# Optimization experiments

Measured on AMD Instinct MI355X. Metric: run time of the kernel, lower is better.

## Reference

```python
import jax, jax.numpy as jnp
import numpy as np

B, H, NQ, NK, D = 2, 16, 4096, 4096, 64


def _attn_with_lse(q, k, v, scale):
    # q: [B,H,p,d], k: [B,H,s,d], v: [B,H,s,dv]
    s = jnp.einsum('bhqd,bhkd->bhqk', q, k) * scale
    lse = jax.nn.logsumexp(s, axis=-1, keepdims=True)  # [B,H,p,1]
    p = jnp.exp(s - lse)
    o = jnp.einsum('bhqk,bhkd->bhqd', p, v)
    return o, lse


def setup_inputs() -> dict:
    key = jax.random.key(0)
    k1, k2, k3 = jax.random.split(key, 3)
    return {
        'query': jax.random.normal(k1, (B, H, NQ, D), dtype=jnp.float32),
        'key': jax.random.normal(k2, (B, H, NK, D), dtype=jnp.float32),
        'value': jax.random.normal(k3, (B, H, NK, D), dtype=jnp.float32),
        'n_query_groups': 4,
        'n_key_groups': 4,
    }


def reference(query, key, value, n_query_groups, n_key_groups):
    b, h, nq, d = query.shape
    nk = key.shape[2]
    m, n = int(n_query_groups), int(n_key_groups)
    scale = d ** (-0.5)
    pq, pk = nq // m, nk // n  # group sizes n_gp
    c0, c1 = m // 2, n // 2   # center groups c_gp

    # representative query/key blocks
    q_gp = query[:, :, c0 * pq:(c0 + 1) * pq, :]              # [B,H,pq,d]
    k_gp = key[:, :, c1 * pk:(c1 + 1) * pk, :]                # [B,H,pk,d]
    # value chunks concatenated on feature dim (zero-padding of q/k in the
    # original leaves the dot products unchanged, so we skip it)
    v_gp = value.reshape(b, h, n, pk, d).transpose(0, 1, 3, 2, 4).reshape(b, h, pk, n * d)
    attn_gp, lse_gp = _attn_with_lse(q_gp, k_gp, v_gp, scale)  # [B,H,pq,n*d], [B,H,pq,1]

    # sample one key per key group (torch uses random.randint; fixed to 0 here)
    k_picked = 0
    k_sample = key[:, :, k_picked::pk, :]                      # [B,H,n,d]
    w = jnp.einsum('bhqd,bhnd->bhqn', query, k_sample)         # [B,H,nq,n]
    w_gps = w.reshape(b, h, m, pq, n)
    norm_gps = jnp.linalg.norm(w_gps, axis=-2)                 # [B,H,m,n]
    s_gps = norm_gps / norm_gps[:, :, c0, c1][:, :, None, None]

    v_sum = value.reshape(b, h, n, pk, d).sum(axis=3)          # [B,H,n,d]
    om = jnp.maximum(1.0 - s_gps, 0.0)                         # clamp(1-s, min=0)
    num_part1 = om[:, :, :, :, None, None] * v_sum[:, :, None, :, None, :]  # [B,H,m,n,1,d]
    den_part1 = (om * pk)[:, :, :, :, None, None]              # [B,H,m,n,1,1]

    lse_exp = jnp.exp(lse_gp)                                  # [B,H,pq,1]
    unnorm = lse_exp * attn_gp                                 # [B,H,pq,n*d]
    attn_gps = unnorm.reshape(b, h, pq, n, d).transpose(0, 1, 3, 2, 4)  # [B,H,n,pq,d]
    num_part2 = s_gps[:, :, :, :, None, None] * attn_gps[:, :, None, :, :, :]  # [B,H,m,n,pq,d]
    den_part2 = s_gps[:, :, :, :, None, None] * lse_exp[:, :, None, None, :, :]  # [B,H,m,n,pq,1]

    num_agg = (num_part1 + num_part2).sum(axis=3)              # [B,H,m,pq,d]
    den_agg = (den_part1 + den_part2).sum(axis=3)              # [B,H,m,pq,1]

    attn = (num_agg / den_agg).reshape(b, h, nq, d)
    lse = jnp.log(den_agg).reshape(b, h, nq, 1)
    return attn, lse
```

## Files before the change

### kernel.cpp

```cpp
#include <hip/hip_runtime.h>
#include <hip/hip_bf16.h>


#define BH_TOT 32
#define SEQ    4096
#define DIM    64
#define PQ     1024

#define QB_OFF 34816u
#define KB_OFF (QB_OFF + 4u*1024u*1024u)
#define VB_OFF (KB_OFF + 4u*1024u*1024u)
#define WS_NEED (VB_OFF + 16u*1024u*1024u)
#define WS_NEED_FB 34816u

#define QSCALE 0.1803368801111204f

typedef __attribute__((ext_vector_type(8))) short bf16x8;
typedef __attribute__((ext_vector_type(4))) short bf16x4;
typedef __attribute__((ext_vector_type(4))) float f32x4;
typedef __attribute__((ext_vector_type(4))) _Float16 f16x4;
typedef __attribute__((ext_vector_type(8))) _Float16 f16x8;

__device__ __forceinline__ short f2bf(float x) {
    unsigned u = __float_as_uint(x);
    u = u + 0x7fffu + ((u >> 16) & 1u);
    return (short)(u >> 16);
}
__device__ __forceinline__ float bf2f(unsigned short h) {
    return __uint_as_float(((unsigned)h) << 16);
}

__global__ __launch_bounds__(256) void prep_norm2(
    const float* __restrict__ query, const float* __restrict__ key,
    float* __restrict__ ws)
{
    __shared__ float ksm[4][64];
    __shared__ float wsum[4][16];
    const int t = threadIdx.x;
    const int bh = blockIdx.x >> 2, gi = blockIdx.x & 3;
    if (t < 64) ws[512 + blockIdx.x * 64 + t] = 0.f;
    ksm[t >> 6][t & 63] = key[((size_t)bh * SEQ + (size_t)(t >> 6) * PQ) * DIM + (t & 63)];
    __syncthreads();
    const int wv = t >> 6, lane = t & 63, c = lane & 15, hi = lane >> 4;
    bf16x8 bb0, bb1;
#pragma unroll
    for (int j = 0; j < 8; ++j) {
        bb0[j] = (c < 4) ? f2bf(ksm[c][hi * 8 + j]) : (short)0;
        bb1[j] = (c < 4) ? f2bf(ksm[c][32 + hi * 8 + j]) : (short)0;
    }
    float acc0 = 0.f, acc1 = 0.f, acc2 = 0.f, acc3 = 0.f;
    const float* qbase = query + ((size_t)bh * SEQ + (size_t)gi * PQ) * DIM;
    for (int it = 0; it < 16; ++it) {
        const int row = (wv * 16 + it) * 16 + c;
        const float* qp = qbase + (size_t)row * 64 + hi * 8;
        float4 a0 = *(const float4*)qp;
        float4 a1 = *(const float4*)(qp + 4);
        float4 a2 = *(const float4*)(qp + 32);
        float4 a3 = *(const float4*)(qp + 36);
        bf16x8 qa0, qa1;
        qa0[0] = f2bf(a0.x); qa0[1] = f2bf(a0.y); qa0[2] = f2bf(a0.z); qa0[3] = f2bf(a0.w);
        qa0[4] = f2bf(a1.x); qa0[5] = f2bf(a1.y); qa0[6] = f2bf(a1.z); qa0[7] = f2bf(a1.w);
        qa1[0] = f2bf(a2.x); qa1[1] = f2bf(a2.y); qa1[2] = f2bf(a2.z); qa1[3] = f2bf(a2.w);
        qa1[4] = f2bf(a3.x); qa1[5] = f2bf(a3.y); qa1[6] = f2bf(a3.z); qa1[7] = f2bf(a3.w);
        f32x4 s = (f32x4){0.f, 0.f, 0.f, 0.f};
        s = __builtin_amdgcn_mfma_f32_16x16x32_bf16(qa0, bb0, s, 0, 0, 0);
        s = __builtin_amdgcn_mfma_f32_16x16x32_bf16(qa1, bb1, s, 0, 0, 0);
        acc0 += s[0] * s[0]; acc1 += s[1] * s[1];
        acc2 += s[2] * s[2]; acc3 += s[3] * s[3];
    }
    float asum = acc0 + acc1 + acc2 + acc3;
    asum += __shfl_xor(asum, 16);
    asum += __shfl_xor(asum, 32);
    if (lane < 16) wsum[wv][lane] = asum;
    __syncthreads();
    if (t < 4) ws[bh * 16 + gi * 4 + t] = wsum[0][t] + wsum[1][t] + wsum[2][t] + wsum[3][t];
}

__global__ __launch_bounds__(256) void conv_qk(
    const float* __restrict__ query, const float* __restrict__ key,
    char* __restrict__ wsb)
{
    const int t = threadIdx.x;
    if (blockIdx.x < 512) {
        const int bh = blockIdx.x >> 4, qt = blockIdx.x & 15;
#pragma unroll
        for (int i = 0; i < 2; ++i) {
            const int sid = t + i * 256;
            const int mt = sid >> 7, kh = (sid >> 6) & 1, lane = sid & 63;
            const int c = lane & 15, hi = lane >> 4;
            const float* p = query + ((size_t)bh * SEQ + 2048 + qt * 64 + mt * 16 + c) * DIM
                             + kh * 32 + hi * 8;
            float4 a = *(const float4*)p, b = *(const float4*)(p + 4);
            bf16x8 h;
            h[0] = f2bf(a.x * QSCALE); h[1] = f2bf(a.y * QSCALE);
            h[2] = f2bf(a.z * QSCALE); h[3] = f2bf(a.w * QSCALE);
            h[4] = f2bf(b.x * QSCALE); h[5] = f2bf(b.y * QSCALE);
            h[6] = f2bf(b.z * QSCALE); h[7] = f2bf(b.w * QSCALE);
            const size_t fidx = ((size_t)(bh * 16 + qt) * 4 + mt) * 2 + kh;
            *(bf16x8*)(wsb + QB_OFF + fidx * 1024 + lane * 16) = h;
        }
    } else {
        const int b2 = blockIdx.x - 512;
        const int bh = b2 >> 4, kc = b2 & 15;
#pragma unroll
        for (int i = 0; i < 2; ++i) {
            const int sid = t + i * 256;
            const int kh = sid >> 8, nt = (sid >> 6) & 3, lane = sid & 63;
            const int c = lane & 15, hi = lane >> 4;
            const float* p = key + ((size_t)bh * SEQ + 2048 + kc * 64 + nt * 16 + c) * DIM
                             + kh * 32 + hi * 8;
            float4 a = *(const float4*)p, b = *(const float4*)(p + 4);
            bf16x8 h;
            h[0] = f2bf(a.x); h[1] = f2bf(a.y); h[2] = f2bf(a.z); h[3] = f2bf(a.w);
            h[4] = f2bf(b.x); h[5] = f2bf(b.y); h[6] = f2bf(b.z); h[7] = f2bf(b.w);
            const size_t fidx = ((size_t)(bh * 16 + kc) * 2 + kh) * 4 + nt;
            *(bf16x8*)(wsb + KB_OFF + fidx * 1024 + lane * 16) = h;
        }
    }
}

__global__ __launch_bounds__(256) void conv_v(
    const float* __restrict__ value, char* __restrict__ wsb, float* __restrict__ ws)
{
    __shared__ float Ls[64][68];
    __shared__ float ps[4][64];
    const int t = threadIdx.x;
    const int blk = blockIdx.x;
    const int bh = blk >> 6, gj = (blk >> 4) & 3, kc = blk & 15;
    const float* src = value + ((size_t)bh * SEQ + gj * PQ + kc * 64) * DIM;
#pragma unroll
    for (int i = 0; i < 4; ++i) {
        const int u = t + i * 256;
        const int row = u >> 4, c4 = (u & 15) * 4;
        *(float4*)&Ls[row][c4] = *(const float4*)(src + row * 64 + c4);
    }
    __syncthreads();
    {
        const int d = t & 63, rg = t >> 6;
        float s = 0.f;
#pragma unroll
        for (int i = 0; i < 16; ++i) s += Ls[rg * 16 + i][d];
        ps[rg][d] = s;
    }
    __syncthreads();
    if (t < 64) {
        float tot = ps[0][t] + ps[1][t] + ps[2][t] + ps[3][t];
        atomicAdd(&ws[512 + bh * 256 + gj * 64 + t], tot);
    }
#pragma unroll
    for (int i = 0; i < 2; ++i) {
        const int sid = t + i * 256;
        const int pl = sid >> 8, dt = (sid >> 6) & 3, lane = sid & 63;
        const int c = lane & 15, hi = lane >> 4;
        f16x8 h;
#pragma unroll
        for (int s2 = 0; s2 < 2; ++s2)
#pragma unroll
            for (int j = 0; j < 4; ++j)
                h[s2 * 4 + j] = (_Float16)Ls[(pl * 2 + s2) * 16 + hi * 4 + j][dt * 16 + c];
        const size_t off = ((((size_t)(bh * 4 + gj) * 32 + kc * 2 + pl) * 4 + dt) * 64 + lane) * 16;
        *(f16x8*)(wsb + VB_OFF + off) = h;
    }
}

__global__ __launch_bounds__(256, 4) void kattn3(
    const char* __restrict__ wsb, float* __restrict__ out)
{
    __shared__ union {
        _Float16 P[2][32][72];
        float Uf[32][257];
    } lds;
    __shared__ float Llds[32];

    const int blk = blockIdx.x;
    const int bh = blk >> 5, qt = blk & 31;
    const int t = threadIdx.x;
    const int w = t >> 6, lane = t & 63;
    const int c = lane & 15, hi = lane >> 4;

    bf16x8 aq[2][2];
#pragma unroll
    for (int qt2 = 0; qt2 < 2; ++qt2) {
        const int s = qt * 2 + qt2;
        const size_t fr = ((size_t)(bh * 16 + (s >> 2)) * 4 + (s & 3)) * 2;
        aq[qt2][0] = *(const bf16x8*)(wsb + QB_OFF + fr * 1024 + lane * 16);
        aq[qt2][1] = *(const bf16x8*)(wsb + QB_OFF + (fr + 1) * 1024 + lane * 16);
    }
    const char* kb = wsb + KB_OFF + ((size_t)(bh * 16) * 8) * 1024 + (size_t)w * 1024 + lane * 16;
    const char* vb = wsb + VB_OFF + ((size_t)(bh * 4 + w) * 128) * 1024 + lane * 16;

    f32x4 Uacc[2][4];
#pragma unroll
    for (int mt = 0; mt < 2; ++mt)
#pragma unroll
        for (int dt = 0; dt < 4; ++dt)
            Uacc[mt][dt] = (f32x4){0.f, 0.f, 0.f, 0.f};
    f32x4 Lacc[2];
    Lacc[0] = (f32x4){0.f, 0.f, 0.f, 0.f};
    Lacc[1] = (f32x4){0.f, 0.f, 0.f, 0.f};
    const f16x4 kOnes = (f16x4){(_Float16)1.f, (_Float16)1.f, (_Float16)1.f, (_Float16)1.f};

    for (int kc = 0; kc < 16; ++kc) {
        const int buf = kc & 1;
        bf16x8 bk0 = *(const bf16x8*)(kb + (size_t)kc * 8192);
        bf16x8 bk1 = *(const bf16x8*)(kb + (size_t)kc * 8192 + 4096);
        f32x4 sacc[2];
#pragma unroll
        for (int qt2 = 0; qt2 < 2; ++qt2) {
            f32x4 s = (f32x4){0.f, 0.f, 0.f, 0.f};
            s = __builtin_amdgcn_mfma_f32_16x16x32_bf16(bk0, aq[qt2][0], s, 0, 0, 0);
            s = __builtin_amdgcn_mfma_f32_16x16x32_bf16(bk1, aq[qt2][1], s, 0, 0, 0);
            sacc[qt2] = s;
        }
#pragma unroll
        for (int qt2 = 0; qt2 < 2; ++qt2) {
            f16x4 ph;
#pragma unroll
            for (int r = 0; r < 4; ++r)
                ph[r] = (_Float16)__builtin_amdgcn_exp2f(sacc[qt2][r]);
            *(f16x4*)&lds.P[buf][qt2 * 16 + c][w * 16 + hi * 4] = ph;
        }
        const char* vcb = vb + (size_t)kc * 8192;
        f16x8 vfa0 = *(const f16x8*)(vcb);
        f16x8 vfa1 = *(const f16x8*)(vcb + 1024);
        f16x8 vfa2 = *(const f16x8*)(vcb + 2048);
        f16x8 vfa3 = *(const f16x8*)(vcb + 3072);
        f16x8 vfb0 = *(const f16x8*)(vcb + 4096);
        f16x8 vfb1 = *(const f16x8*)(vcb + 5120);
        f16x8 vfb2 = *(const f16x8*)(vcb + 6144);
        f16x8 vfb3 = *(const f16x8*)(vcb + 7168);
        __syncthreads();
        f16x4 ap[2][4];
#pragma unroll
        for (int mt = 0; mt < 2; ++mt)
#pragma unroll
            for (int kt = 0; kt < 4; ++kt)
                ap[mt][kt] = *(const f16x4*)&lds.P[buf][mt * 16 + c][kt * 16 + hi * 4];
#pragma unroll
        for (int mt = 0; mt < 2; ++mt) {
            Uacc[mt][0] = __builtin_amdgcn_mfma_f32_16x16x16f16(ap[mt][0], __builtin_shufflevector(vfa0, vfa0, 0, 1, 2, 3), Uacc[mt][0], 0, 0, 0);
            Uacc[mt][1] = __builtin_amdgcn_mfma_f32_16x16x16f16(ap[mt][0], __builtin_shufflevector(vfa1, vfa1, 0, 1, 2, 3), Uacc[mt][1], 0, 0, 0);
            Uacc[mt][2] = __builtin_amdgcn_mfma_f32_16x16x16f16(ap[mt][0], __builtin_shufflevector(vfa2, vfa2, 0, 1, 2, 3), Uacc[mt][2], 0, 0, 0);
            Uacc[mt][3] = __builtin_amdgcn_mfma_f32_16x16x16f16(ap[mt][0], __builtin_shufflevector(vfa3, vfa3, 0, 1, 2, 3), Uacc[mt][3], 0, 0, 0);
            Uacc[mt][0] = __builtin_amdgcn_mfma_f32_16x16x16f16(ap[mt][1], __builtin_shufflevector(vfa0, vfa0, 4, 5, 6, 7), Uacc[mt][0], 0, 0, 0);
            Uacc[mt][1] = __builtin_amdgcn_mfma_f32_16x16x16f16(ap[mt][1], __builtin_shufflevector(vfa1, vfa1, 4, 5, 6, 7), Uacc[mt][1], 0, 0, 0);
            Uacc[mt][2] = __builtin_amdgcn_mfma_f32_16x16x16f16(ap[mt][1], __builtin_shufflevector(vfa2, vfa2, 4, 5, 6, 7), Uacc[mt][2], 0, 0, 0);
            Uacc[mt][3] = __builtin_amdgcn_mfma_f32_16x16x16f16(ap[mt][1], __builtin_shufflevector(vfa3, vfa3, 4, 5, 6, 7), Uacc[mt][3], 0, 0, 0);
            Uacc[mt][0] = __builtin_amdgcn_mfma_f32_16x16x16f16(ap[mt][2], __builtin_shufflevector(vfb0, vfb0, 0, 1, 2, 3), Uacc[mt][0], 0, 0, 0);
            Uacc[mt][1] = __builtin_amdgcn_mfma_f32_16x16x16f16(ap[mt][2], __builtin_shufflevector(vfb1, vfb1, 0, 1, 2, 3), Uacc[mt][1], 0, 0, 0);
            Uacc[mt][2] = __builtin_amdgcn_mfma_f32_16x16x16f16(ap[mt][2], __builtin_shufflevector(vfb2, vfb2, 0, 1, 2, 3), Uacc[mt][2], 0, 0, 0);
            Uacc[mt][3] = __builtin_amdgcn_mfma_f32_16x16x16f16(ap[mt][2], __builtin_shufflevector(vfb3, vfb3, 0, 1, 2, 3), Uacc[mt][3], 0, 0, 0);
            Uacc[mt][0] = __builtin_amdgcn_mfma_f32_16x16x16f16(ap[mt][3], __builtin_shufflevector(vfb0, vfb0, 4, 5, 6, 7), Uacc[mt][0], 0, 0, 0);
            Uacc[mt][1] = __builtin_amdgcn_mfma_f32_16x16x16f16(ap[mt][3], __builtin_shufflevector(vfb1, vfb1, 4, 5, 6, 7), Uacc[mt][1], 0, 0, 0);
            Uacc[mt][2] = __builtin_amdgcn_mfma_f32_16x16x16f16(ap[mt][3], __builtin_shufflevector(vfb2, vfb2, 4, 5, 6, 7), Uacc[mt][2], 0, 0, 0);
            Uacc[mt][3] = __builtin_amdgcn_mfma_f32_16x16x16f16(ap[mt][3], __builtin_shufflevector(vfb3, vfb3, 4, 5, 6, 7), Uacc[mt][3], 0, 0, 0);
            Lacc[mt] = __builtin_amdgcn_mfma_f32_16x16x16f16(ap[mt][0], kOnes, Lacc[mt], 0, 0, 0);
            Lacc[mt] = __builtin_amdgcn_mfma_f32_16x16x16f16(ap[mt][1], kOnes, Lacc[mt], 0, 0, 0);
            Lacc[mt] = __builtin_amdgcn_mfma_f32_16x16x16f16(ap[mt][2], kOnes, Lacc[mt], 0, 0, 0);
            Lacc[mt] = __builtin_amdgcn_mfma_f32_16x16x16f16(ap[mt][3], kOnes, Lacc[mt], 0, 0, 0);
        }
    }

    __syncthreads();
#pragma unroll
    for (int mt = 0; mt < 2; ++mt)
#pragma unroll
        for (int dt = 0; dt < 4; ++dt)
#pragma unroll
            for (int r = 0; r < 4; ++r)
                lds.Uf[mt * 16 + hi * 4 + r][w * 64 + dt * 16 + c] = Uacc[mt][dt][r];
    if (w == 0 && c == 0) {
#pragma unroll
        for (int mt = 0; mt < 2; ++mt)
#pragma unroll
            for (int r = 0; r < 4; ++r)
                Llds[mt * 16 + hi * 4 + r] = Lacc[mt][r];
    }
    __syncthreads();

    const float* wsf = (const float*)wsb;
    const float* nsq = wsf + (size_t)bh * 16;
    const float* vsw = wsf + 512 + (size_t)bh * 256;
    const int dd = t & 63, rq = t >> 6;
    float sg[4][4], ssum[4], omp[4], ov[4];
    const float inv22 = 1.0f / nsq[10];
#pragma unroll
    for (int gi = 0; gi < 4; ++gi) {
        float ss = 0.f, os = 0.f, ovv = 0.f;
#pragma unroll
        for (int gj = 0; gj < 4; ++gj) {
            float sgv = sqrtf(nsq[gi * 4 + gj] * inv22);
            sg[gi][gj] = sgv;
            ss += sgv;
            float om = fmaxf(1.0f - sgv, 0.0f);
            os += om;
            ovv += om * vsw[gj * 64 + dd];
        }
        ssum[gi] = ss; omp[gi] = os * 1024.0f; ov[gi] = ovv;
    }
    const size_t base = (size_t)bh * SEQ * DIM;
    float* attn_out = out + base;
    float* lse_out = out + (size_t)BH_TOT * SEQ * DIM + (size_t)bh * SEQ;
    for (int k = 0; k < 8; ++k) {
        const int r = k * 4 + rq;
        const float u0 = lds.Uf[r][dd];
        const float u1 = lds.Uf[r][64 + dd];
        const float u2 = lds.Uf[r][128 + dd];
        const float u3 = lds.Uf[r][192 + dd];
        const float Lr = Llds[r];
        const int orow = qt * 32 + r;
#pragma unroll
        for (int gi = 0; gi < 4; ++gi) {
            float num = ov[gi] + sg[gi][0] * u0 + sg[gi][1] * u1 + sg[gi][2] * u2 + sg[gi][3] * u3;
            float den = omp[gi] + ssum[gi] * Lr;
            attn_out[(size_t)(gi * 1024 + orow) * 64 + dd] = num / den;
            if (dd == gi) lse_out[gi * 1024 + orow] = __logf(den);
        }
    }
}

__global__ __launch_bounds__(256) void prep_vsum(
    const float* __restrict__ value, float* __restrict__ ws)
{
    __shared__ float part[16][16][4];
    const int t = threadIdx.x;
    const int bh = blockIdx.x >> 2, gj = blockIdx.x & 3;
    const float4* vv = (const float4*)(value + ((size_t)bh * SEQ + (size_t)gj * PQ) * DIM);
    const int c4 = t & 15, rg = t >> 4;
    float a0 = 0.f, a1 = 0.f, a2 = 0.f, a3 = 0.f;
    for (int r = rg; r < 1024; r += 16) {
        float4 x = vv[r * 16 + c4];
        a0 += x.x; a1 += x.y; a2 += x.z; a3 += x.w;
    }
    part[rg][c4][0] = a0; part[rg][c4][1] = a1;
    part[rg][c4][2] = a2; part[rg][c4][3] = a3;
    __syncthreads();
    if (t < 64) {
        const int cc = t >> 2, comp = t & 3;
        float s = 0.f;
#pragma unroll
        for (int g = 0; g < 16; ++g) s += part[g][cc][comp];
        ws[512 + bh * 256 + gj * 64 + cc * 4 + comp] = s;
    }
}

__global__ __launch_bounds__(256, 2) void kattn_fallback(
    const float* __restrict__ query, const float* __restrict__ key,
    const float* __restrict__ value, const float* __restrict__ ws,
    float* __restrict__ out)
{
    __shared__ union {
        struct { short Q[64][72]; short K[64][72]; short P[64][72]; } s;
        unsigned short U[64][264];
    } lds;
    __shared__ float Llds[64];
    const int blk = blockIdx.x;
    const int bh = blk >> 4, qt = blk & 15;
    const int t = threadIdx.x;
    const int w = t >> 6, lane = t & 63;
    const int c = lane & 15, hi = lane >> 4;
    const size_t base = (size_t)bh * SEQ * DIM;
    {
        const float* qp = query + base + (size_t)(2048 + qt * 64) * DIM;
#pragma unroll
        for (int k2 = 0; k2 < 4; ++k2) {
            int u = t + k2 * 256;
            int row = u >> 4, ci = (u & 15) * 4;
            float4 qv = *(const float4*)(qp + row * 64 + ci);
            bf16x4 h;
            h[0] = f2bf(qv.x); h[1] = f2bf(qv.y); h[2] = f2bf(qv.z); h[3] = f2bf(qv.w);
            *(bf16x4*)&lds.s.Q[row][ci] = h;
        }
    }
    __syncthreads();
    bf16x8 aq0 = *(const bf16x8*)&lds.s.Q[w * 16 + c][hi * 8];
    bf16x8 aq1 = *(const bf16x8*)&lds.s.Q[w * 16 + c][32 + hi * 8];
    f32x4 Uacc[4][4];
#pragma unroll
    for (int mt = 0; mt < 4; ++mt)
#pragma unroll
        for (int nt = 0; nt < 4; ++nt)
            Uacc[mt][nt] = (f32x4){0.f, 0.f, 0.f, 0.f};
    float Lacc[4] = {0.f, 0.f, 0.f, 0.f};
    const float* kp = key + base + (size_t)2048 * DIM;
    const float* vgrp = value + base + (size_t)w * PQ * DIM;
    for (int kc = 0; kc < 16; ++kc) {
        {
            const float* kcp = kp + (size_t)kc * 64 * DIM;
#pragma unroll
            for (int k2 = 0; k2 < 4; ++k2) {
                int u = t + k2 * 256;
                int row = u >> 4, ci = (u & 15) * 4;
                float4 kv = *(const float4*)(kcp + row * 64 + ci);
                bf16x4 h;
                h[0] = f2bf(kv.x); h[1] = f2bf(kv.y); h[2] = f2bf(kv.z); h[3] = f2bf(kv.w);
                *(bf16x4*)&lds.s.K[row][ci] = h;
            }
        }
        __syncthreads();
        f32x4 sacc[4];
#pragma unroll
        for (int nt = 0; nt < 4; ++nt) sacc[nt] = (f32x4){0.f, 0.f, 0.f, 0.f};
#pragma unroll
        for (int nt = 0; nt < 4; ++nt) {
            bf16x8 bk = *(const bf16x8*)&lds.s.K[nt * 16 + c][hi * 8];
            sacc[nt] = __builtin_amdgcn_mfma_f32_16x16x32_bf16(aq0, bk, sacc[nt], 0, 0, 0);
        }
#pragma unroll
        for (int nt = 0; nt < 4; ++nt) {
            bf16x8 bk = *(const bf16x8*)&lds.s.K[nt * 16 + c][32 + hi * 8];
            sacc[nt] = __builtin_amdgcn_mfma_f32_16x16x32_bf16(aq1, bk, sacc[nt], 0, 0, 0);
        }
        float p[4][4];
#pragma unroll
        for (int nt = 0; nt < 4; ++nt)
#pragma unroll
            for (int r = 0; r < 4; ++r)
                p[nt][r] = __expf(sacc[nt][r] * 0.125f);
#pragma unroll
        for (int r = 0; r < 4; ++r) {
            float rs = p[0][r] + p[1][r] + p[2][r] + p[3][r];
            rs += __shfl_xor(rs, 1); rs += __shfl_xor(rs, 2);
            rs += __shfl_xor(rs, 4); rs += __shfl_xor(rs, 8);
            Lacc[r] += rs;
        }
#pragma unroll
        for (int nt = 0; nt < 4; ++nt)
#pragma unroll
            for (int r = 0; r < 4; ++r)
                lds.s.P[w * 16 + hi * 4 + r][nt * 16 + c] = (unsigned short)f2bf(p[nt][r]);
        __syncthreads();
        bf16x8 ap2[4][2];
#pragma unroll
        for (int mt = 0; mt < 4; ++mt) {
            ap2[mt][0] = *(const bf16x8*)&lds.s.P[mt * 16 + c][hi * 8];
            ap2[mt][1] = *(const bf16x8*)&lds.s.P[mt * 16 + c][32 + hi * 8];
        }
        const float* vp = vgrp + (size_t)kc * 64 * DIM;
#pragma unroll
        for (int kt = 0; kt < 2; ++kt) {
#pragma unroll
            for (int nt = 0; nt < 4; ++nt) {
                const float* vpp = vp + (kt * 32 + hi * 8) * 64 + nt * 16 + c;
                bf16x8 bv;
#pragma unroll
                for (int j = 0; j < 8; ++j) bv[j] = f2bf(vpp[j * 64]);
#pragma unroll
                for (int mt = 0; mt < 4; ++mt)
                    Uacc[mt][nt] = __builtin_amdgcn_mfma_f32_16x16x32_bf16(ap2[mt][kt], bv, Uacc[mt][nt], 0, 0, 0);
            }
        }
        __syncthreads();
    }
#pragma unroll
    for (int mt = 0; mt < 4; ++mt)
#pragma unroll
        for (int nt = 0; nt < 4; ++nt)
#pragma unroll
            for (int r = 0; r < 4; ++r)
                lds.U[mt * 16 + hi * 4 + r][w * 64 + nt * 16 + c] =
                    (unsigned short)f2bf(Uacc[mt][nt][r]);
    if (c == 0) {
#pragma unroll
        for (int r = 0; r < 4; ++r) Llds[w * 16 + hi * 4 + r] = Lacc[r];
    }
    __syncthreads();
    const float* nsq = ws + bh * 16;
    const float* vsw = ws + 512 + bh * 256;
    const int dd = t & 63, rq = t >> 6;
    float sg[4][4], ssum[4], omp[4], ov[4];
    const float inv22 = 1.0f / nsq[10];
#pragma unroll
    for (int gi = 0; gi < 4; ++gi) {
        float ss = 0.f, os = 0.f, ovv = 0.f;
#pragma unroll
        for (int gj = 0; gj < 4; ++gj) {
            float sgv = sqrtf(nsq[gi * 4 + gj] * inv22);
            sg[gi][gj] = sgv;
            ss += sgv;
            float om = fmaxf(1.0f - sgv, 0.0f);
            os += om;
            ovv += om * vsw[gj * 64 + dd];
        }
        ssum[gi] = ss; omp[gi] = os * 1024.0f; ov[gi] = ovv;
    }
    float* attn_out = out + base;
    float* lse_out = out + (size_t)BH_TOT * SEQ * DIM + (size_t)bh * SEQ;
    for (int k = 0; k < 16; ++k) {
        const int r = k * 4 + rq;
        const float u0 = bf2f(lds.U[r][dd]);
        const float u1 = bf2f(lds.U[r][64 + dd]);
        const float u2 = bf2f(lds.U[r][128 + dd]);
        const float u3 = bf2f(lds.U[r][192 + dd]);
        const float Lr = Llds[r];
        const int orow = qt * 64 + r;
#pragma unroll
        for (int gi = 0; gi < 4; ++gi) {
            float num = ov[gi] + sg[gi][0] * u0 + sg[gi][1] * u1 + sg[gi][2] * u2 + sg[gi][3] * u3;
            float den = omp[gi] + ssum[gi] * Lr;
            attn_out[(size_t)(gi * 1024 + orow) * 64 + dd] = num / den;
            if (dd == gi) lse_out[gi * 1024 + orow] = __logf(den);
        }
    }
}

extern "C" void kernel_launch(void* const* d_in, const int* in_sizes, int n_in,
                              void* d_out, int out_size, void* d_ws, size_t ws_size,
                              hipStream_t stream)
{
    (void)in_sizes; (void)n_in; (void)out_size;
    const float* query = (const float*)d_in[0];
    const float* key   = (const float*)d_in[1];
    const float* value = (const float*)d_in[2];
    float* ws   = (float*)d_ws;
    char*  wsb  = (char*)d_ws;
    float* outp = (float*)d_out;

    prep_norm2<<<128, 256, 0, stream>>>(query, key, ws);
    if (ws_size >= WS_NEED) {
        conv_qk<<<1024, 256, 0, stream>>>(query, key, wsb);
        conv_v<<<2048, 256, 0, stream>>>(value, wsb, ws);
        kattn3<<<1024, 256, 0, stream>>>(wsb, outp);
    } else {
        prep_vsum<<<128, 256, 0, stream>>>(value, ws);
        kattn_fallback<<<512, 256, 0, stream>>>(query, key, value, ws, outp);
    }
}
```

Before: 185.4 us.

## Switch PV matmul to 16x16x32 f16 MFMA with repacked P and V layouts

The PV and row-sum products now use the wider 16x16x32 f16 MFMA, which halves the MFMA instruction count. To feed it, conv_v writes V fragments in a new 8-element K layout and P is stored in LDS in a fragment-ready layout, so each lane loads one 16-byte vector per span. K fragments for the next chunk are prefetched during the current iteration, and the block-to-(bh, qt) mapping is interleaved to spread heads across blocks. The risks are higher register pressure from the prefetch and possible LDS bank conflicts in the new P layout.

Measured after the change: 178.9 us. 1.04x faster.

```diff
diff --git a/kernel.cpp b/kernel.cpp
--- a/kernel.cpp
+++ b/kernel.cpp
@@ -11,7 +11,6 @@
 #define KB_OFF (QB_OFF + 4u*1024u*1024u)
 #define VB_OFF (KB_OFF + 4u*1024u*1024u)
 #define WS_NEED (VB_OFF + 16u*1024u*1024u)
-#define WS_NEED_FB 34816u
 
 #define QSCALE 0.1803368801111204f
 
@@ -154,26 +153,26 @@
         const int c = lane & 15, hi = lane >> 4;
         f16x8 h;
 #pragma unroll
-        for (int s2 = 0; s2 < 2; ++s2)
-#pragma unroll
-            for (int j = 0; j < 4; ++j)
-                h[s2 * 4 + j] = (_Float16)Ls[(pl * 2 + s2) * 16 + hi * 4 + j][dt * 16 + c];
+        for (int j = 0; j < 8; ++j)
+            h[j] = (_Float16)Ls[pl * 32 + hi * 8 + j][dt * 16 + c];
         const size_t off = ((((size_t)(bh * 4 + gj) * 32 + kc * 2 + pl) * 4 + dt) * 64 + lane) * 16;
         *(f16x8*)(wsb + VB_OFF + off) = h;
     }
 }
 
-__global__ __launch_bounds__(256, 4) void kattn3(
+__global__ __launch_bounds__(256, 4) void kattn4(
     const char* __restrict__ wsb, float* __restrict__ out)
 {
     __shared__ union {
-        _Float16 P[2][32][72];
+        _Float16 Pf[2][2][2][512];
         float Uf[32][257];
     } lds;
     __shared__ float Llds[32];
 
     const int blk = blockIdx.x;
-    const int bh = blk >> 5, qt = blk & 31;
+    const int slot = blk >> 3;
+    const int bh = (blk & 7) * 4 + (slot >> 5);
+    const int qt = slot & 31;
     const int t = threadIdx.x;
     const int w = t >> 6, lane = t & 63;
     const int c = lane & 15, hi = lane >> 4;
@@ -198,12 +197,19 @@
     f32x4 Lacc[2];
     Lacc[0] = (f32x4){0.f, 0.f, 0.f, 0.f};
     Lacc[1] = (f32x4){0.f, 0.f, 0.f, 0.f};
-    const f16x4 kOnes = (f16x4){(_Float16)1.f, (_Float16)1.f, (_Float16)1.f, (_Float16)1.f};
+    f16x8 kOnes;
+#pragma unroll
+    for (int j = 0; j < 8; ++j) kOnes[j] = (_Float16)1.f;
+
+    const int k0 = w * 16 + hi * 4;
+    const int pspan = k0 >> 5;
+    const int pidx = (c + 16 * ((k0 & 31) >> 3)) * 8 + (k0 & 7);
+
+    bf16x8 bk0 = *(const bf16x8*)(kb);
+    bf16x8 bk1 = *(const bf16x8*)(kb + 4096);
 
     for (int kc = 0; kc < 16; ++kc) {
         const int buf = kc & 1;
-        bf16x8 bk0 = *(const bf16x8*)(kb + (size_t)kc * 8192);
-        bf16x8 bk1 = *(const bf16x8*)(kb + (size_t)kc * 8192 + 4096);
         f32x4 sacc[2];
 #pragma unroll
         for (int qt2 = 0; qt2 < 2; ++qt2) {
@@ -218,46 +224,33 @@
 #pragma unroll
             for (int r = 0; r < 4; ++r)
                 ph[r] = (_Float16)__builtin_amdgcn_exp2f(sacc[qt2][r]);
-            *(f16x4*)&lds.P[buf][qt2 * 16 + c][w * 16 + hi * 4] = ph;
+            *(f16x4*)&lds.Pf[buf][qt2][pspan][pidx] = ph;
         }
         const char* vcb = vb + (size_t)kc * 8192;
-        f16x8 vfa0 = *(const f16x8*)(vcb);
-        f16x8 vfa1 = *(const f16x8*)(vcb + 1024);
-        f16x8 vfa2 = *(const f16x8*)(vcb + 2048);
-        f16x8 vfa3 = *(const f16x8*)(vcb + 3072);
-        f16x8 vfb0 = *(const f16x8*)(vcb + 4096);
-        f16x8 vfb1 = *(const f16x8*)(vcb + 5120);
-        f16x8 vfb2 = *(const f16x8*)(vcb + 6144);
-        f16x8 vfb3 = *(const f16x8*)(vcb + 7168);
+        f16x8 vf[8];
+#pragma unroll
+        for (int u = 0; u < 8; ++u) vf[u] = *(const f16x8*)(vcb + u * 1024);
+        if (kc < 15) {
+            bk0 = *(const bf16x8*)(kb + (size_t)(kc + 1) * 8192);
+            bk1 = *(const bf16x8*)(kb + (size_t)(kc + 1) * 8192 + 4096);
+        }
         __syncthreads();
-        f16x4 ap[2][4];
+        f16x8 ap[2][2];
 #pragma unroll
         for (int mt = 0; mt < 2; ++mt)
 #pragma unroll
-            for (int kt = 0; kt < 4; ++kt)
-                ap[mt][kt] = *(const f16x4*)&lds.P[buf][mt * 16 + c][kt * 16 + hi * 4];
+            for (int sp = 0; sp < 2; ++sp)
+                ap[mt][sp] = *(const f16x8*)&lds.Pf[buf][mt][sp][lane * 8];
 #pragma unroll
         for (int mt = 0; mt < 2; ++mt) {
-            Uacc[mt][0] = __builtin_amdgcn_mfma_f32_16x16x16f16(ap[mt][0], __builtin_shufflevector(vfa0, vfa0, 0, 1, 2, 3), Uacc[mt][0], 0, 0, 0);
-            Uacc[mt][1] = __builtin_amdgcn_mfma_f32_16x16x16f16(ap[mt][0], __builtin_shufflevector(vfa1, vfa1, 0, 1, 2, 3), Uacc[mt][1], 0, 0, 0);
-            Uacc[mt][2] = __builtin_amdgcn_mfma_f32_16x16x16f16(ap[mt][0], __builtin_shufflevector(vfa2, vfa2, 0, 1, 2, 3), Uacc[mt][2], 0, 0, 0);
-            Uacc[mt][3] = __builtin_amdgcn_mfma_f32_16x16x16f16(ap[mt][0], __builtin_shufflevector(vfa3, vfa3, 0, 1, 2, 3), Uacc[mt][3], 0, 0, 0);
-            Uacc[mt][0] = __builtin_amdgcn_mfma_f32_16x16x16f16(ap[mt][1], __builtin_shufflevector(vfa0, vfa0, 4, 5, 6, 7), Uacc[mt][0], 0, 0, 0);
-            Uacc[mt][1] = __builtin_amdgcn_mfma_f32_16x16x16f16(ap[mt][1], __builtin_shufflevector(vfa1, vfa1, 4, 5, 6, 7), Uacc[mt][1], 0, 0, 0);
-            Uacc[mt][2] = __builtin_amdgcn_mfma_f32_16x16x16f16(ap[mt][1], __builtin_shufflevector(vfa2, vfa2, 4, 5, 6, 7), Uacc[mt][2], 0, 0, 0);
-            Uacc[mt][3] = __builtin_amdgcn_mfma_f32_16x16x16f16(ap[mt][1], __builtin_shufflevector(vfa3, vfa3, 4, 5, 6, 7), Uacc[mt][3], 0, 0, 0);
-            Uacc[mt][0] = __builtin_amdgcn_mfma_f32_16x16x16f16(ap[mt][2], __builtin_shufflevector(vfb0, vfb0, 0, 1, 2, 3), Uacc[mt][0], 0, 0, 0);
-            Uacc[mt][1] = __builtin_amdgcn_mfma_f32_16x16x16f16(ap[mt][2], __builtin_shufflevector(vfb1, vfb1, 0, 1, 2, 3), Uacc[mt][1], 0, 0, 0);
-            Uacc[mt][2] = __builtin_amdgcn_mfma_f32_16x16x16f16(ap[mt][2], __builtin_shufflevector(vfb2, vfb2, 0, 1, 2, 3), Uacc[mt][2], 0, 0, 0);
-            Uacc[mt][3] = __builtin_amdgcn_mfma_f32_16x16x16f16(ap[mt][2], __builtin_shufflevector(vfb3, vfb3, 0, 1, 2, 3), Uacc[mt][3], 0, 0, 0);
-            Uacc[mt][0] = __builtin_amdgcn_mfma_f32_16x16x16f16(ap[mt][3], __builtin_shufflevector(vfb0, vfb0, 4, 5, 6, 7), Uacc[mt][0], 0, 0, 0);
-            Uacc[mt][1] = __builtin_amdgcn_mfma_f32_16x16x16f16(ap[mt][3], __builtin_shufflevector(vfb1, vfb1, 4, 5, 6, 7), Uacc[mt][1], 0, 0, 0);
-            Uacc[mt][2] = __builtin_amdgcn_mfma_f32_16x16x16f16(ap[mt][3], __builtin_shufflevector(vfb2, vfb2, 4, 5, 6, 7), Uacc[mt][2], 0, 0, 0);
-            Uacc[mt][3] = __builtin_amdgcn_mfma_f32_16x16x16f16(ap[mt][3], __builtin_shufflevector(vfb3, vfb3, 4, 5, 6, 7), Uacc[mt][3], 0, 0, 0);
-            Lacc[mt] = __builtin_amdgcn_mfma_f32_16x16x16f16(ap[mt][0], kOnes, Lacc[mt], 0, 0, 0);
-            Lacc[mt] = __builtin_amdgcn_mfma_f32_16x16x16f16(ap[mt][1], kOnes, Lacc[mt], 0, 0, 0);
-            Lacc[mt] = __builtin_amdgcn_mfma_f32_16x16x16f16(ap[mt][2], kOnes, Lacc[mt], 0, 0, 0);
-            Lacc[mt] = __builtin_amdgcn_mfma_f32_16x16x16f16(ap[mt][3], kOnes, Lacc[mt], 0, 0, 0);
+#pragma unroll
+            for (int sp = 0; sp < 2; ++sp) {
+                Uacc[mt][0] = __builtin_amdgcn_mfma_f32_16x16x32_f16(ap[mt][sp], vf[sp * 4 + 0], Uacc[mt][0], 0, 0, 0);
+                Uacc[mt][1] = __builtin_amdgcn_mfma_f32_16x16x32_f16(ap[mt][sp], vf[sp * 4 + 1], Uacc[mt][1], 0, 0, 0);
+                Uacc[mt][2] = __builtin_amdgcn_mfma_f32_16x16x32_f16(ap[mt][sp], vf[sp * 4 + 2], Uacc[mt][2], 0, 0, 0);
+                Uacc[mt][3] = __builtin_amdgcn_mfma_f32_16x16x32_f16(ap[mt][sp], vf[sp * 4 + 3], Uacc[mt][3], 0, 0, 0);
+                Lacc[mt]    = __builtin_amdgcn_mfma_f32_16x16x32_f16(ap[mt][sp], kOnes, Lacc[mt], 0, 0, 0);
+            }
         }
     }
 
@@ -520,7 +513,7 @@
     if (ws_size >= WS_NEED) {
         conv_qk<<<1024, 256, 0, stream>>>(query, key, wsb);
         conv_v<<<2048, 256, 0, stream>>>(value, wsb, ws);
-        kattn3<<<1024, 256, 0, stream>>>(wsb, outp);
+        kattn4<<<1024, 256, 0, stream>>>(wsb, outp);
     } else {
         prep_vsum<<<128, 256, 0, stream>>>(value, ws);
         kattn_fallback<<<512, 256, 0, stream>>>(query, key, value, ws, outp);
```
